# Kernel optimization log

Measured on AMD Instinct MI355X. Metric: run time of the kernel, lower is better.

Reference implementation:

```python
import jax, jax.numpy as jnp
import numpy as np
import math

EPS_T = 1e-3   # temperature floor from `sigmoid(raw)*(1-0.001)+0.001`
EPS_W = 1e-8   # normalization epsilon


def _cdist(a, b):
    # Euclidean distance matrix [N, C], like torch.cdist(p=2).
    a2 = jnp.sum(a * a, axis=-1, keepdims=True)        # [N, 1]
    b2 = jnp.sum(b * b, axis=-1)                       # [C]
    d2 = a2 + b2 - 2.0 * (a @ b.T)                     # [N, C]
    return jnp.sqrt(jnp.maximum(d2, 1e-12))


def setup_inputs() -> dict:
    key = jax.random.key(0)
    k_x, k_p, k_g = jax.random.split(key, 3)
    N, D, C = 262144, 128, 256
    x = jax.random.normal(k_x, (N, D), dtype=jnp.float32)
    prototypes = jax.random.normal(k_p, (C, D), dtype=jnp.float32)
    grid_pos = jax.random.normal(k_g, (C, D), dtype=jnp.float32)
    # logit(0.95) so temperature == init_temperature
    temp_raw = jnp.array([math.log(0.95 / 0.05)], dtype=jnp.float32)
    gate_logits = jnp.zeros((C,), dtype=jnp.float32)
    return {"x": x, "prototypes": prototypes, "grid_pos": grid_pos,
            "temp_raw": temp_raw, "gate_logits": gate_logits}


def reference(x, prototypes, grid_pos, temp_raw, gate_logits):
    temperature = jax.nn.sigmoid(temp_raw)[0] * (1.0 - EPS_T) + EPS_T
    gate = jax.nn.sigmoid(gate_logits)[None, :]            # [1, C]
    d_total = _cdist(x, prototypes) + _cdist(x, grid_pos)  # [N, C]
    w = jnp.exp(-d_total / temperature)
    w = w / (jnp.sum(w, axis=-1, keepdims=True) + EPS_W)
    w = w * gate
    w = w / (jnp.sum(w, axis=-1, keepdims=True) + EPS_W)
    blended = w @ prototypes                               # [N, D]
    return blended, w
```

## Files before the change

### kernel.cpp

```cpp
#include <hip/hip_runtime.h>

typedef short v8s __attribute__((ext_vector_type(8)));
typedef float v4f __attribute__((ext_vector_type(4)));
typedef float f32x16 __attribute__((ext_vector_type(16)));
typedef unsigned int v2u __attribute__((ext_vector_type(2)));
typedef unsigned int v4u __attribute__((ext_vector_type(4)));
typedef unsigned short ushort_t;

#define NC 256
#define ND 128

__device__ __forceinline__ unsigned short f2bf(float f) {
  union { float f; unsigned int u; } v; v.f = f;
  unsigned int u = v.u;
  unsigned int r = (u + 0x7fffu + ((u >> 16) & 1u)) >> 16;
  return (unsigned short)r;
}

__device__ __forceinline__ unsigned int cvt_pk_bf16(float a, float b) {
  unsigned int r;
  asm("v_cvt_pk_bf16_f32 %0, %1, %2" : "=v"(r) : "v"(a), "v"(b));
  return r;
}

__device__ __forceinline__ float bf_lo(unsigned int u) { return __uint_as_float(u << 16); }
__device__ __forceinline__ float bf_hi(unsigned int u) { return __uint_as_float(u & 0xffff0000u); }

__global__ void som_prep_kernel(const float* __restrict__ P, const float* __restrict__ G,
                                const float* __restrict__ gate_logits,
                                ushort_t* __restrict__ PbfA, ushort_t* __restrict__ GbfA,
                                ushort_t* __restrict__ PTbfA,
                                float* __restrict__ b2p, float* __restrict__ b2g,
                                float* __restrict__ gatev) {
  int c = blockIdx.x;
  int t = threadIdx.x;
  float p = P[c * ND + t];
  float g = G[c * ND + t];

  int ct = c >> 5, l31 = c & 31;
  int s = t >> 4, hia = (t >> 3) & 1, j = t & 7;
  int lane = l31 + 32 * hia;
  PbfA[((ct * 8 + s) * 64 + lane) * 8 + j] = f2bf(p);
  GbfA[((ct * 8 + s) * 64 + lane) * 8 + j] = f2bf(g);

  int dt = t >> 5, l31d = t & 31;
  int sc = c >> 4, hic = (c >> 3) & 1, jc = c & 7;
  int laned = l31d + 32 * hic;
  PTbfA[((dt * 16 + sc) * 64 + laned) * 8 + jc] = f2bf(p);

  float pp = p * p, gg = g * g;
  #pragma unroll
  for (int m = 1; m < 64; m <<= 1) { pp += __shfl_xor(pp, m); gg += __shfl_xor(gg, m); }
  __shared__ float sp[2], sg[2];
  if ((t & 63) == 0) { sp[t >> 6] = pp; sg[t >> 6] = gg; }
  __syncthreads();
  if (t == 0) {
    b2p[c] = sp[0] + sp[1];
    b2g[c] = sg[0] + sg[1];
    gatev[c] = 1.f / (1.f + expf(-gate_logits[c]));
  }
}

__global__ __launch_bounds__(256, 2) void som_main_kernel(
    const float* __restrict__ x,
    const ushort_t* __restrict__ PbfA,
    const ushort_t* __restrict__ GbfA,
    const ushort_t* __restrict__ PTbfA,
    const float* __restrict__ b2p,
    const float* __restrict__ b2g,
    const float* __restrict__ gatev,
    const float* __restrict__ temp_raw,
    float* __restrict__ blended_out,
    float* __restrict__ w_out)
{
  __shared__ char smem[65536];
  const int tid  = threadIdx.x;
  const int wid  = tid >> 6;
  const int lane = tid & 63;
  const int l31  = lane & 31;
  const int hi   = lane >> 5;
  const long long R = ((long long)blockIdx.x * 4 + wid) * 32;
  char* wl = smem + wid * 16384;
  const int rsw = (l31 & 7) << 4;

  float traw = temp_raw[0];
  float sgm = 1.f / (1.f + __builtin_amdgcn_exp2f(-traw * 1.44269504f));
  float T = sgm * (1.f - 1e-3f) + 1e-3f;
  float k2 = 1.44269504f / T;

  const float* xr = x + (R + l31) * ND + hi * 8;
  v8s xb[8];
  float a2 = 0.f;
  #pragma unroll
  for (int s = 0; s < 8; ++s) {
    v4f lo = *(const v4f*)(xr + s * 16);
    v4f h4 = *(const v4f*)(xr + s * 16 + 4);
    v4u w;
    w[0] = cvt_pk_bf16(lo[0], lo[1]);
    w[1] = cvt_pk_bf16(lo[2], lo[3]);
    w[2] = cvt_pk_bf16(h4[0], h4[1]);
    w[3] = cvt_pk_bf16(h4[2], h4[3]);
    xb[s] = __builtin_bit_cast(v8s, w);
    #pragma unroll
    for (int j = 0; j < 4; ++j) {
      a2 = fmaf(lo[j], lo[j], a2);
      a2 = fmaf(h4[j], h4[j], a2);
    }
  }
  a2 += __shfl_xor(a2, 32);

  float s1 = 0.f, su = 0.f;
  const ushort_t* pb = PbfA + lane * 8;
  const ushort_t* gb = GbfA + lane * 8;
  #pragma unroll
  for (int ct = 0; ct < 8; ++ct) {
    f32x16 aP, aG;
    #pragma unroll
    for (int i = 0; i < 16; ++i) { aP[i] = 0.f; aG[i] = 0.f; }
    #pragma unroll
    for (int s = 0; s < 8; ++s) {
      v8s ap = *(const v8s*)(pb + (ct * 8 + s) * 512);
      v8s ag = *(const v8s*)(gb + (ct * 8 + s) * 512);
      aP = __builtin_amdgcn_mfma_f32_32x32x16_bf16(ap, xb[s], aP, 0, 0, 0);
      aG = __builtin_amdgcn_mfma_f32_32x32x16_bf16(ag, xb[s], aG, 0, 0, 0);
    }
    #pragma unroll
    for (int q = 0; q < 4; ++q) {
      int c0 = ct * 32 + q * 8 + hi * 4;
      v4f bp = *(const v4f*)(b2p + c0);
      v4f bg = *(const v4f*)(b2g + c0);
      v4f gt = *(const v4f*)(gatev + c0);
      float uf[4];
      #pragma unroll
      for (int j2 = 0; j2 < 4; ++j2) {
        int r = q * 4 + j2;
        float d2a = fmaf(-2.f, aP[r], a2 + bp[j2]);
        float d2b = fmaf(-2.f, aG[r], a2 + bg[j2]);
        float d = __builtin_amdgcn_sqrtf(fmaxf(d2a, 1e-12f))
                + __builtin_amdgcn_sqrtf(fmaxf(d2b, 1e-12f));
        float e = __builtin_amdgcn_exp2f(-d * k2);
        float uu = e * gt[j2];
        s1 += e; su += uu;
        uf[j2] = uu;
      }
      v2u pk;
      pk[0] = cvt_pk_bf16(uf[0], uf[1]);
      pk[1] = cvt_pk_bf16(uf[2], uf[3]);
      *(v2u*)(wl + l31 * 512 + ((ct * 64 + q * 16 + hi * 8) ^ rsw)) = pk;
    }
  }
  s1 += __shfl_xor(s1, 32);
  su += __shfl_xor(su, 32);
  float scale = 1.f / (su + 1e-8f * (s1 + 1e-8f));

  #pragma unroll
  for (int p = 0; p < 4; ++p) {
    int row = (lane >> 3) + 8 * p;
    float rsc = __shfl(scale, row);
    float* wdst = w_out + (size_t)(R + row) * NC + (lane & 7) * 4;
    #pragma unroll
    for (int ch = 0; ch < 8; ++ch) {
      v2u pk = *(const v2u*)(wl + row * 512 + ((ch * 64 + (lane & 7) * 8) ^ ((row & 7) << 4)));
      v4f wv;
      wv[0] = bf_lo(pk[0]) * rsc;
      wv[1] = bf_hi(pk[0]) * rsc;
      wv[2] = bf_lo(pk[1]) * rsc;
      wv[3] = bf_hi(pk[1]) * rsc;
      *(v4f*)(wdst + ch * 32) = wv;
    }
  }

  f32x16 acc[4];
  #pragma unroll
  for (int dt = 0; dt < 4; ++dt)
    #pragma unroll
    for (int i = 0; i < 16; ++i) acc[dt][i] = 0.f;

  const ushort_t* tb = PTbfA + lane * 8;
  #pragma unroll
  for (int s2 = 0; s2 < 16; ++s2) {
    v4u bw = *(const v4u*)(wl + l31 * 512 + ((s2 * 32 + hi * 16) ^ rsw));
    v8s bfrag = __builtin_bit_cast(v8s, bw);
    #pragma unroll
    for (int dt = 0; dt < 4; ++dt) {
      v8s pa = *(const v8s*)(tb + (dt * 16 + s2) * 512);
      acc[dt] = __builtin_amdgcn_mfma_f32_32x32x16_bf16(pa, bfrag, acc[dt], 0, 0, 0);
    }
  }

  #pragma unroll
  for (int dt = 0; dt < 4; ++dt) {
    #pragma unroll
    for (int q = 0; q < 4; ++q) {
      v4f ov;
      ov[0] = acc[dt][4 * q + 0] * scale;
      ov[1] = acc[dt][4 * q + 1] * scale;
      ov[2] = acc[dt][4 * q + 2] * scale;
      ov[3] = acc[dt][4 * q + 3] * scale;
      *(v4f*)(wl + l31 * 512 + ((dt * 128 + q * 32 + hi * 16) ^ rsw)) = ov;
    }
  }
  #pragma unroll
  for (int p = 0; p < 4; ++p) {
    int row = (lane >> 3) + 8 * p;
    float* bdst = blended_out + (size_t)(R + row) * ND + (lane & 7) * 4;
    #pragma unroll
    for (int ch = 0; ch < 4; ++ch) {
      v4f bv = *(const v4f*)(wl + row * 512 + ((ch * 128 + (lane & 7) * 16) ^ ((row & 7) << 4)));
      *(v4f*)(bdst + ch * 32) = bv;
    }
  }
}

extern "C" void kernel_launch(void* const* d_in, const int* in_sizes, int n_in,
                              void* d_out, int out_size, void* d_ws, size_t ws_size,
                              hipStream_t stream) {
  const float* x    = (const float*)d_in[0];
  const float* P    = (const float*)d_in[1];
  const float* G    = (const float*)d_in[2];
  const float* traw = (const float*)d_in[3];
  const float* gl   = (const float*)d_in[4];
  const int N = in_sizes[0] / ND;

  char* ws = (char*)d_ws;
  ushort_t* PbfA  = (ushort_t*)(ws);
  ushort_t* GbfA  = (ushort_t*)(ws + 65536);
  ushort_t* PTbfA = (ushort_t*)(ws + 131072);
  float* b2p   = (float*)(ws + 196608);
  float* b2g   = (float*)(ws + 197632);
  float* gatev = (float*)(ws + 198656);

  float* blended = (float*)d_out;
  float* wout    = blended + (size_t)N * ND;

  som_prep_kernel<<<NC, ND, 0, stream>>>(P, G, gl, PbfA, GbfA, PTbfA, b2p, b2g, gatev);
  som_main_kernel<<<N / 128, 256, 0, stream>>>(x, PbfA, GbfA, PTbfA, b2p, b2g, gatev,
                                               traw, blended, wout);
}
```

Measured before the change: 152.3 us.

## Switch to 16x16x32 MFMA tiles with 16 rows per wave for higher occupancy

```diff
diff --git a/kernel.cpp b/kernel.cpp
--- a/kernel.cpp
+++ b/kernel.cpp
@@ -2,13 +2,13 @@
 
 typedef short v8s __attribute__((ext_vector_type(8)));
 typedef float v4f __attribute__((ext_vector_type(4)));
-typedef float f32x16 __attribute__((ext_vector_type(16)));
 typedef unsigned int v2u __attribute__((ext_vector_type(2)));
 typedef unsigned int v4u __attribute__((ext_vector_type(4)));
 typedef unsigned short ushort_t;
 
 #define NC 256
 #define ND 128
+#define ROW_B 528
 
 __device__ __forceinline__ unsigned short f2bf(float f) {
   union { float f; unsigned int u; } v; v.f = f;
@@ -37,16 +37,20 @@
   float p = P[c * ND + t];
   float g = G[c * ND + t];
 
-  int ct = c >> 5, l31 = c & 31;
-  int s = t >> 4, hia = (t >> 3) & 1, j = t & 7;
-  int lane = l31 + 32 * hia;
-  PbfA[((ct * 8 + s) * 64 + lane) * 8 + j] = f2bf(p);
-  GbfA[((ct * 8 + s) * 64 + lane) * 8 + j] = f2bf(g);
-
-  int dt = t >> 5, l31d = t & 31;
-  int sc = c >> 4, hic = (c >> 3) & 1, jc = c & 7;
-  int laned = l31d + 32 * hic;
-  PTbfA[((dt * 16 + sc) * 64 + laned) * 8 + jc] = f2bf(p);
+  {
+    int ct = c >> 4, l15 = c & 15;
+    int s = t >> 5, q4 = (t >> 3) & 3, j = t & 7;
+    int lane = l15 + 16 * q4;
+    int idx = ((ct * 4 + s) * 64 + lane) * 8 + j;
+    PbfA[idx] = f2bf(p);
+    GbfA[idx] = f2bf(g);
+  }
+  {
+    int dt = t >> 4, l15 = t & 15;
+    int s2 = c >> 5, q4 = (c >> 3) & 3, j = c & 7;
+    int lane = l15 + 16 * q4;
+    PTbfA[((dt * 8 + s2) * 64 + lane) * 8 + j] = f2bf(p);
+  }
 
   float pp = p * p, gg = g * g;
   #pragma unroll
@@ -61,7 +65,7 @@
   }
 }
 
-__global__ __launch_bounds__(256, 2) void som_main_kernel(
+__global__ __launch_bounds__(256, 4) void som_main_kernel(
     const float* __restrict__ x,
     const ushort_t* __restrict__ PbfA,
     const ushort_t* __restrict__ GbfA,
@@ -73,28 +77,27 @@
     float* __restrict__ blended_out,
     float* __restrict__ w_out)
 {
-  __shared__ char smem[65536];
+  __shared__ char smem[4 * 16 * ROW_B];
   const int tid  = threadIdx.x;
   const int wid  = tid >> 6;
   const int lane = tid & 63;
-  const int l31  = lane & 31;
-  const int hi   = lane >> 5;
-  const long long R = ((long long)blockIdx.x * 4 + wid) * 32;
-  char* wl = smem + wid * 16384;
-  const int rsw = (l31 & 7) << 4;
+  const int l15  = lane & 15;
+  const int q4   = lane >> 4;
+  const long long R = ((long long)blockIdx.x * 4 + wid) * 16;
+  char* wl = smem + wid * 16 * ROW_B;
 
   float traw = temp_raw[0];
   float sgm = 1.f / (1.f + __builtin_amdgcn_exp2f(-traw * 1.44269504f));
   float T = sgm * (1.f - 1e-3f) + 1e-3f;
   float k2 = 1.44269504f / T;
 
-  const float* xr = x + (R + l31) * ND + hi * 8;
-  v8s xb[8];
+  const float* xr = x + (R + l15) * ND + q4 * 8;
+  v8s xb[4];
   float a2 = 0.f;
   #pragma unroll
-  for (int s = 0; s < 8; ++s) {
-    v4f lo = *(const v4f*)(xr + s * 16);
-    v4f h4 = *(const v4f*)(xr + s * 16 + 4);
+  for (int s = 0; s < 4; ++s) {
+    v4f lo = *(const v4f*)(xr + s * 32);
+    v4f h4 = *(const v4f*)(xr + s * 32 + 4);
     v4u w;
     w[0] = cvt_pk_bf16(lo[0], lo[1]);
     w[1] = cvt_pk_bf16(lo[2], lo[3]);
@@ -107,108 +110,94 @@
       a2 = fmaf(h4[j], h4[j], a2);
     }
   }
+  a2 += __shfl_xor(a2, 16);
   a2 += __shfl_xor(a2, 32);
 
   float s1 = 0.f, su = 0.f;
   const ushort_t* pb = PbfA + lane * 8;
   const ushort_t* gb = GbfA + lane * 8;
   #pragma unroll
-  for (int ct = 0; ct < 8; ++ct) {
-    f32x16 aP, aG;
-    #pragma unroll
-    for (int i = 0; i < 16; ++i) { aP[i] = 0.f; aG[i] = 0.f; }
-    #pragma unroll
-    for (int s = 0; s < 8; ++s) {
-      v8s ap = *(const v8s*)(pb + (ct * 8 + s) * 512);
-      v8s ag = *(const v8s*)(gb + (ct * 8 + s) * 512);
-      aP = __builtin_amdgcn_mfma_f32_32x32x16_bf16(ap, xb[s], aP, 0, 0, 0);
-      aG = __builtin_amdgcn_mfma_f32_32x32x16_bf16(ag, xb[s], aG, 0, 0, 0);
-    }
-    #pragma unroll
-    for (int q = 0; q < 4; ++q) {
-      int c0 = ct * 32 + q * 8 + hi * 4;
-      v4f bp = *(const v4f*)(b2p + c0);
-      v4f bg = *(const v4f*)(b2g + c0);
-      v4f gt = *(const v4f*)(gatev + c0);
-      float uf[4];
-      #pragma unroll
-      for (int j2 = 0; j2 < 4; ++j2) {
-        int r = q * 4 + j2;
-        float d2a = fmaf(-2.f, aP[r], a2 + bp[j2]);
-        float d2b = fmaf(-2.f, aG[r], a2 + bg[j2]);
-        float d = __builtin_amdgcn_sqrtf(fmaxf(d2a, 1e-12f))
-                + __builtin_amdgcn_sqrtf(fmaxf(d2b, 1e-12f));
-        float e = __builtin_amdgcn_exp2f(-d * k2);
-        float uu = e * gt[j2];
-        s1 += e; su += uu;
-        uf[j2] = uu;
-      }
-      v2u pk;
-      pk[0] = cvt_pk_bf16(uf[0], uf[1]);
-      pk[1] = cvt_pk_bf16(uf[2], uf[3]);
-      *(v2u*)(wl + l31 * 512 + ((ct * 64 + q * 16 + hi * 8) ^ rsw)) = pk;
-    }
-  }
-  s1 += __shfl_xor(s1, 32);
-  su += __shfl_xor(su, 32);
+  for (int ct = 0; ct < 16; ++ct) {
+    v4f aP = {0.f,0.f,0.f,0.f}, aG = {0.f,0.f,0.f,0.f};
+    #pragma unroll
+    for (int s = 0; s < 4; ++s) {
+      v8s ap = *(const v8s*)(pb + (ct * 4 + s) * 512);
+      v8s ag = *(const v8s*)(gb + (ct * 4 + s) * 512);
+      aP = __builtin_amdgcn_mfma_f32_16x16x32_bf16(ap, xb[s], aP, 0, 0, 0);
+      aG = __builtin_amdgcn_mfma_f32_16x16x32_bf16(ag, xb[s], aG, 0, 0, 0);
+    }
+    int c0 = ct * 16 + q4 * 4;
+    v4f bp = *(const v4f*)(b2p + c0);
+    v4f bg = *(const v4f*)(b2g + c0);
+    v4f gt = *(const v4f*)(gatev + c0);
+    float uf[4];
+    #pragma unroll
+    for (int r = 0; r < 4; ++r) {
+      float d2a = fmaf(-2.f, aP[r], a2 + bp[r]);
+      float d2b = fmaf(-2.f, aG[r], a2 + bg[r]);
+      float d = __builtin_amdgcn_sqrtf(fmaxf(d2a, 1e-12f))
+              + __builtin_amdgcn_sqrtf(fmaxf(d2b, 1e-12f));
+      float e = __builtin_amdgcn_exp2f(-d * k2);
+      float uu = e * gt[r];
+      s1 += e; su += uu;
+      uf[r] = uu;
+    }
+    v2u pk;
+    pk[0] = cvt_pk_bf16(uf[0], uf[1]);
+    pk[1] = cvt_pk_bf16(uf[2], uf[3]);
+    *(v2u*)(wl + l15 * ROW_B + ct * 32 + q4 * 8) = pk;
+  }
+  s1 += __shfl_xor(s1, 16); s1 += __shfl_xor(s1, 32);
+  su += __shfl_xor(su, 16); su += __shfl_xor(su, 32);
   float scale = 1.f / (su + 1e-8f * (s1 + 1e-8f));
 
-  #pragma unroll
-  for (int p = 0; p < 4; ++p) {
-    int row = (lane >> 3) + 8 * p;
-    float rsc = __shfl(scale, row);
-    float* wdst = w_out + (size_t)(R + row) * NC + (lane & 7) * 4;
-    #pragma unroll
-    for (int ch = 0; ch < 8; ++ch) {
-      v2u pk = *(const v2u*)(wl + row * 512 + ((ch * 64 + (lane & 7) * 8) ^ ((row & 7) << 4)));
-      v4f wv;
-      wv[0] = bf_lo(pk[0]) * rsc;
-      wv[1] = bf_hi(pk[0]) * rsc;
-      wv[2] = bf_lo(pk[1]) * rsc;
-      wv[3] = bf_hi(pk[1]) * rsc;
-      *(v4f*)(wdst + ch * 32) = wv;
-    }
-  }
-
-  f32x16 acc[4];
-  #pragma unroll
-  for (int dt = 0; dt < 4; ++dt)
-    #pragma unroll
-    for (int i = 0; i < 16; ++i) acc[dt][i] = 0.f;
-
+  const int erow = lane >> 2;
+  const int ek   = lane & 3;
+  float rsc = __shfl(scale, erow);
+  float* wdst = w_out + (size_t)(R + erow) * NC + ek * 8;
+  #pragma unroll
+  for (int ch = 0; ch < 8; ++ch) {
+    v4u pk = *(const v4u*)(wl + erow * ROW_B + ch * 64 + ek * 16);
+    v4f w0, w1;
+    w0[0] = bf_lo(pk[0]) * rsc; w0[1] = bf_hi(pk[0]) * rsc;
+    w0[2] = bf_lo(pk[1]) * rsc; w0[3] = bf_hi(pk[1]) * rsc;
+    w1[0] = bf_lo(pk[2]) * rsc; w1[1] = bf_hi(pk[2]) * rsc;
+    w1[2] = bf_lo(pk[3]) * rsc; w1[3] = bf_hi(pk[3]) * rsc;
+    *(v4f*)(wdst + ch * 32)     = w0;
+    *(v4f*)(wdst + ch * 32 + 4) = w1;
+  }
+
+  v4f acc[8];
+  #pragma unroll
+  for (int dt = 0; dt < 8; ++dt) acc[dt] = (v4f){0.f,0.f,0.f,0.f};
   const ushort_t* tb = PTbfA + lane * 8;
   #pragma unroll
-  for (int s2 = 0; s2 < 16; ++s2) {
-    v4u bw = *(const v4u*)(wl + l31 * 512 + ((s2 * 32 + hi * 16) ^ rsw));
+  for (int s2 = 0; s2 < 8; ++s2) {
+    v4u bw = *(const v4u*)(wl + l15 * ROW_B + s2 * 64 + q4 * 16);
     v8s bfrag = __builtin_bit_cast(v8s, bw);
     #pragma unroll
-    for (int dt = 0; dt < 4; ++dt) {
-      v8s pa = *(const v8s*)(tb + (dt * 16 + s2) * 512);
-      acc[dt] = __builtin_amdgcn_mfma_f32_32x32x16_bf16(pa, bfrag, acc[dt], 0, 0, 0);
-    }
-  }
-
-  #pragma unroll
-  for (int dt = 0; dt < 4; ++dt) {
-    #pragma unroll
-    for (int q = 0; q < 4; ++q) {
-      v4f ov;
-      ov[0] = acc[dt][4 * q + 0] * scale;
-      ov[1] = acc[dt][4 * q + 1] * scale;
-      ov[2] = acc[dt][4 * q + 2] * scale;
-      ov[3] = acc[dt][4 * q + 3] * scale;
-      *(v4f*)(wl + l31 * 512 + ((dt * 128 + q * 32 + hi * 16) ^ rsw)) = ov;
-    }
-  }
-  #pragma unroll
-  for (int p = 0; p < 4; ++p) {
-    int row = (lane >> 3) + 8 * p;
-    float* bdst = blended_out + (size_t)(R + row) * ND + (lane & 7) * 4;
-    #pragma unroll
-    for (int ch = 0; ch < 4; ++ch) {
-      v4f bv = *(const v4f*)(wl + row * 512 + ((ch * 128 + (lane & 7) * 16) ^ ((row & 7) << 4)));
-      *(v4f*)(bdst + ch * 32) = bv;
-    }
+    for (int dt = 0; dt < 8; ++dt) {
+      v8s pa = *(const v8s*)(tb + (dt * 8 + s2) * 512);
+      acc[dt] = __builtin_amdgcn_mfma_f32_16x16x32_bf16(pa, bfrag, acc[dt], 0, 0, 0);
+    }
+  }
+
+  #pragma unroll
+  for (int dt = 0; dt < 8; ++dt) {
+    v4f ov;
+    ov[0] = acc[dt][0] * scale;
+    ov[1] = acc[dt][1] * scale;
+    ov[2] = acc[dt][2] * scale;
+    ov[3] = acc[dt][3] * scale;
+    *(v4f*)(wl + l15 * ROW_B + dt * 64 + q4 * 16) = ov;
+  }
+  float* bdst = blended_out + (size_t)(R + erow) * ND + ek * 8;
+  #pragma unroll
+  for (int ch = 0; ch < 4; ++ch) {
+    v4f b0 = *(const v4f*)(wl + erow * ROW_B + ch * 128 + ek * 32);
+    v4f b1 = *(const v4f*)(wl + erow * ROW_B + ch * 128 + ek * 32 + 16);
+    *(v4f*)(bdst + ch * 32)     = b0;
+    *(v4f*)(bdst + ch * 32 + 4) = b1;
   }
 }
 
@@ -234,6 +223,6 @@
   float* wout    = blended + (size_t)N * ND;
 
   som_prep_kernel<<<NC, ND, 0, stream>>>(P, G, gl, PbfA, GbfA, PTbfA, b2p, b2g, gatev);
-  som_main_kernel<<<N / 128, 256, 0, stream>>>(x, PbfA, GbfA, PTbfA, b2p, b2g, gatev,
-                                               traw, blended, wout);
-}
+  som_main_kernel<<<N / 64, 256, 0, stream>>>(x, PbfA, GbfA, PTbfA, b2p, b2g, gatev,
+                                              traw, blended, wout);
+}
```

After: 211.3 us. +38.7%, slower.

## Split each 32-row tile across a wave pair to double waves per block

Applied to the files above, without the earlier changes.

```diff
diff --git a/kernel.cpp b/kernel.cpp
--- a/kernel.cpp
+++ b/kernel.cpp
@@ -61,7 +61,7 @@
   }
 }
 
-__global__ __launch_bounds__(256, 2) void som_main_kernel(
+__global__ __launch_bounds__(512, 4) void som_main_kernel(
     const float* __restrict__ x,
     const ushort_t* __restrict__ PbfA,
     const ushort_t* __restrict__ GbfA,
@@ -73,14 +73,17 @@
     float* __restrict__ blended_out,
     float* __restrict__ w_out)
 {
-  __shared__ char smem[65536];
+  __shared__ char smem[4 * 16384 + 2048];
   const int tid  = threadIdx.x;
   const int wid  = tid >> 6;
+  const int pair = wid >> 1;
+  const int h    = wid & 1;
   const int lane = tid & 63;
   const int l31  = lane & 31;
   const int hi   = lane >> 5;
-  const long long R = ((long long)blockIdx.x * 4 + wid) * 32;
-  char* wl = smem + wid * 16384;
+  const long long R = ((long long)blockIdx.x * 4 + pair) * 32;
+  char* wl = smem + pair * 16384;
+  float* sums = (float*)(smem + 65536) + pair * 128;
   const int rsw = (l31 & 7) << 4;
 
   float traw = temp_raw[0];
@@ -113,7 +116,8 @@
   const ushort_t* pb = PbfA + lane * 8;
   const ushort_t* gb = GbfA + lane * 8;
   #pragma unroll
-  for (int ct = 0; ct < 8; ++ct) {
+  for (int ct8 = 0; ct8 < 4; ++ct8) {
+    const int ct = h * 4 + ct8;
     f32x16 aP, aG;
     #pragma unroll
     for (int i = 0; i < 16; ++i) { aP[i] = 0.f; aG[i] = 0.f; }
@@ -151,11 +155,19 @@
   }
   s1 += __shfl_xor(s1, 32);
   su += __shfl_xor(su, 32);
-  float scale = 1.f / (su + 1e-8f * (s1 + 1e-8f));
-
-  #pragma unroll
-  for (int p = 0; p < 4; ++p) {
-    int row = (lane >> 3) + 8 * p;
+  if (hi == 0) {
+    sums[h * 64 + l31]      = s1;
+    sums[h * 64 + 32 + l31] = su;
+  }
+  __syncthreads();
+
+  float s1t = sums[l31] + sums[64 + l31];
+  float sut = sums[32 + l31] + sums[96 + l31];
+  float scale = 1.f / (sut + 1e-8f * (s1t + 1e-8f));
+
+  #pragma unroll
+  for (int pp = 0; pp < 2; ++pp) {
+    int row = (lane >> 3) + 8 * (2 * h + pp);
     float rsc = __shfl(scale, row);
     float* wdst = w_out + (size_t)(R + row) * NC + (lane & 7) * 4;
     #pragma unroll
@@ -170,11 +182,11 @@
     }
   }
 
-  f32x16 acc[4];
-  #pragma unroll
-  for (int dt = 0; dt < 4; ++dt)
-    #pragma unroll
-    for (int i = 0; i < 16; ++i) acc[dt][i] = 0.f;
+  f32x16 acc[2];
+  #pragma unroll
+  for (int dt2 = 0; dt2 < 2; ++dt2)
+    #pragma unroll
+    for (int i = 0; i < 16; ++i) acc[dt2][i] = 0.f;
 
   const ushort_t* tb = PTbfA + lane * 8;
   #pragma unroll
@@ -182,27 +194,32 @@
     v4u bw = *(const v4u*)(wl + l31 * 512 + ((s2 * 32 + hi * 16) ^ rsw));
     v8s bfrag = __builtin_bit_cast(v8s, bw);
     #pragma unroll
-    for (int dt = 0; dt < 4; ++dt) {
-      v8s pa = *(const v8s*)(tb + (dt * 16 + s2) * 512);
-      acc[dt] = __builtin_amdgcn_mfma_f32_32x32x16_bf16(pa, bfrag, acc[dt], 0, 0, 0);
-    }
-  }
-
-  #pragma unroll
-  for (int dt = 0; dt < 4; ++dt) {
+    for (int dt2 = 0; dt2 < 2; ++dt2) {
+      int dtg = h * 2 + dt2;
+      v8s pa = *(const v8s*)(tb + (dtg * 16 + s2) * 512);
+      acc[dt2] = __builtin_amdgcn_mfma_f32_32x32x16_bf16(pa, bfrag, acc[dt2], 0, 0, 0);
+    }
+  }
+  __syncthreads();
+
+  #pragma unroll
+  for (int dt2 = 0; dt2 < 2; ++dt2) {
+    int dtg = h * 2 + dt2;
     #pragma unroll
     for (int q = 0; q < 4; ++q) {
       v4f ov;
-      ov[0] = acc[dt][4 * q + 0] * scale;
-      ov[1] = acc[dt][4 * q + 1] * scale;
-      ov[2] = acc[dt][4 * q + 2] * scale;
-      ov[3] = acc[dt][4 * q + 3] * scale;
-      *(v4f*)(wl + l31 * 512 + ((dt * 128 + q * 32 + hi * 16) ^ rsw)) = ov;
-    }
-  }
-  #pragma unroll
-  for (int p = 0; p < 4; ++p) {
-    int row = (lane >> 3) + 8 * p;
+      ov[0] = acc[dt2][4 * q + 0] * scale;
+      ov[1] = acc[dt2][4 * q + 1] * scale;
+      ov[2] = acc[dt2][4 * q + 2] * scale;
+      ov[3] = acc[dt2][4 * q + 3] * scale;
+      *(v4f*)(wl + l31 * 512 + ((dtg * 128 + q * 32 + hi * 16) ^ rsw)) = ov;
+    }
+  }
+  __syncthreads();
+
+  #pragma unroll
+  for (int pp = 0; pp < 2; ++pp) {
+    int row = (lane >> 3) + 8 * (2 * h + pp);
     float* bdst = blended_out + (size_t)(R + row) * ND + (lane & 7) * 4;
     #pragma unroll
     for (int ch = 0; ch < 4; ++ch) {
@@ -234,6 +251,6 @@
   float* wout    = blended + (size_t)N * ND;
 
   som_prep_kernel<<<NC, ND, 0, stream>>>(P, G, gl, PbfA, GbfA, PTbfA, b2p, b2g, gatev);
-  som_main_kernel<<<N / 128, 256, 0, stream>>>(x, PbfA, GbfA, PTbfA, b2p, b2g, gatev,
+  som_main_kernel<<<N / 128, 512, 0, stream>>>(x, PbfA, GbfA, PTbfA, b2p, b2g, gatev,
                                                traw, blended, wout);
 }
```

Measured after the change: 165.3 us. +8.5%, slower.

## Recompute distance GEMM in two passes to shrink LDS and raise occupancy

Applied to the files above, without the earlier changes.

```diff
diff --git a/kernel.cpp b/kernel.cpp
--- a/kernel.cpp
+++ b/kernel.cpp
@@ -3,12 +3,12 @@
 typedef short v8s __attribute__((ext_vector_type(8)));
 typedef float v4f __attribute__((ext_vector_type(4)));
 typedef float f32x16 __attribute__((ext_vector_type(16)));
-typedef unsigned int v2u __attribute__((ext_vector_type(2)));
 typedef unsigned int v4u __attribute__((ext_vector_type(4)));
 typedef unsigned short ushort_t;
 
 #define NC 256
 #define ND 128
+#define LROW 36
 
 __device__ __forceinline__ unsigned short f2bf(float f) {
   union { float f; unsigned int u; } v; v.f = f;
@@ -23,8 +23,9 @@
   return r;
 }
 
-__device__ __forceinline__ float bf_lo(unsigned int u) { return __uint_as_float(u << 16); }
-__device__ __forceinline__ float bf_hi(unsigned int u) { return __uint_as_float(u & 0xffff0000u); }
+__device__ __forceinline__ void plane32swap(unsigned int &a, unsigned int &b) {
+  asm("v_permlane32_swap_b32 %0, %1" : "+v"(a), "+v"(b));
+}
 
 __global__ void som_prep_kernel(const float* __restrict__ P, const float* __restrict__ G,
                                 const float* __restrict__ gate_logits,
@@ -61,7 +62,7 @@
   }
 }
 
-__global__ __launch_bounds__(256, 2) void som_main_kernel(
+__global__ __launch_bounds__(256, 3) void som_main_kernel(
     const float* __restrict__ x,
     const ushort_t* __restrict__ PbfA,
     const ushort_t* __restrict__ GbfA,
@@ -73,15 +74,16 @@
     float* __restrict__ blended_out,
     float* __restrict__ w_out)
 {
-  __shared__ char smem[65536];
+  __shared__ float smem[4 * 32 * LROW];
   const int tid  = threadIdx.x;
   const int wid  = tid >> 6;
   const int lane = tid & 63;
   const int l31  = lane & 31;
   const int hi   = lane >> 5;
   const long long R = ((long long)blockIdx.x * 4 + wid) * 32;
-  char* wl = smem + wid * 16384;
-  const int rsw = (l31 & 7) << 4;
+  float* wl = smem + wid * 32 * LROW;
+  const int erow = lane >> 3;
+  const int eseg = lane & 7;
 
   float traw = temp_raw[0];
   float sgm = 1.f / (1.f + __builtin_amdgcn_exp2f(-traw * 1.44269504f));
@@ -109,9 +111,10 @@
   }
   a2 += __shfl_xor(a2, 32);
 
-  float s1 = 0.f, su = 0.f;
   const ushort_t* pb = PbfA + lane * 8;
   const ushort_t* gb = GbfA + lane * 8;
+
+  float s1 = 0.f, su = 0.f;
   #pragma unroll
   for (int ct = 0; ct < 8; ++ct) {
     f32x16 aP, aG;
@@ -124,6 +127,58 @@
       aP = __builtin_amdgcn_mfma_f32_32x32x16_bf16(ap, xb[s], aP, 0, 0, 0);
       aG = __builtin_amdgcn_mfma_f32_32x32x16_bf16(ag, xb[s], aG, 0, 0, 0);
     }
+    #pragma unroll
+    for (int q = 0; q < 4; ++q) {
+      int c0 = ct * 32 + q * 8 + hi * 4;
+      v4f bp = *(const v4f*)(b2p + c0);
+      v4f bg = *(const v4f*)(b2g + c0);
+      v4f gt = *(const v4f*)(gatev + c0);
+      #pragma unroll
+      for (int j2 = 0; j2 < 4; ++j2) {
+        int r = q * 4 + j2;
+        float d2a = fmaf(-2.f, aP[r], a2 + bp[j2]);
+        float d2b = fmaf(-2.f, aG[r], a2 + bg[j2]);
+        float d = __builtin_amdgcn_sqrtf(fmaxf(d2a, 1e-12f))
+                + __builtin_amdgcn_sqrtf(fmaxf(d2b, 1e-12f));
+        float e = __builtin_amdgcn_exp2f(-d * k2);
+        s1 += e;
+        su = fmaf(e, gt[j2], su);
+      }
+    }
+  }
+  s1 += __shfl_xor(s1, 32);
+  su += __shfl_xor(su, 32);
+  float scale = 1.f / (su + 1e-8f * (s1 + 1e-8f));
+
+  #pragma unroll
+  for (int s = 0; s < 8; ++s) {
+    v4u t = __builtin_bit_cast(v4u, xb[s]);
+    unsigned int t0 = t[0], t1 = t[1], t2 = t[2], t3 = t[3];
+    asm volatile("" : "+v"(t0), "+v"(t1), "+v"(t2), "+v"(t3));
+    t[0] = t0; t[1] = t1; t[2] = t2; t[3] = t3;
+    xb[s] = __builtin_bit_cast(v8s, t);
+  }
+
+  f32x16 acc[4];
+  #pragma unroll
+  for (int dt = 0; dt < 4; ++dt)
+    #pragma unroll
+    for (int i = 0; i < 16; ++i) acc[dt][i] = 0.f;
+  const ushort_t* tb = PTbfA + lane * 8;
+
+  #pragma unroll
+  for (int ct = 0; ct < 8; ++ct) {
+    f32x16 aP, aG;
+    #pragma unroll
+    for (int i = 0; i < 16; ++i) { aP[i] = 0.f; aG[i] = 0.f; }
+    #pragma unroll
+    for (int s = 0; s < 8; ++s) {
+      v8s ap = *(const v8s*)(pb + (ct * 8 + s) * 512);
+      v8s ag = *(const v8s*)(gb + (ct * 8 + s) * 512);
+      aP = __builtin_amdgcn_mfma_f32_32x32x16_bf16(ap, xb[s], aP, 0, 0, 0);
+      aG = __builtin_amdgcn_mfma_f32_32x32x16_bf16(ag, xb[s], aG, 0, 0, 0);
+    }
+    unsigned int w8[8];
     #pragma unroll
     for (int q = 0; q < 4; ++q) {
       int c0 = ct * 32 + q * 8 + hi * 4;
@@ -139,52 +194,34 @@
         float d = __builtin_amdgcn_sqrtf(fmaxf(d2a, 1e-12f))
                 + __builtin_amdgcn_sqrtf(fmaxf(d2b, 1e-12f));
         float e = __builtin_amdgcn_exp2f(-d * k2);
-        float uu = e * gt[j2];
-        s1 += e; su += uu;
-        uf[j2] = uu;
+        uf[j2] = e * gt[j2];
       }
-      v2u pk;
-      pk[0] = cvt_pk_bf16(uf[0], uf[1]);
-      pk[1] = cvt_pk_bf16(uf[2], uf[3]);
-      *(v2u*)(wl + l31 * 512 + ((ct * 64 + q * 16 + hi * 8) ^ rsw)) = pk;
-    }
-  }
-  s1 += __shfl_xor(s1, 32);
-  su += __shfl_xor(su, 32);
-  float scale = 1.f / (su + 1e-8f * (s1 + 1e-8f));
-
-  #pragma unroll
-  for (int p = 0; p < 4; ++p) {
-    int row = (lane >> 3) + 8 * p;
-    float rsc = __shfl(scale, row);
-    float* wdst = w_out + (size_t)(R + row) * NC + (lane & 7) * 4;
-    #pragma unroll
-    for (int ch = 0; ch < 8; ++ch) {
-      v2u pk = *(const v2u*)(wl + row * 512 + ((ch * 64 + (lane & 7) * 8) ^ ((row & 7) << 4)));
+      w8[2 * q]     = cvt_pk_bf16(uf[0], uf[1]);
+      w8[2 * q + 1] = cvt_pk_bf16(uf[2], uf[3]);
       v4f wv;
-      wv[0] = bf_lo(pk[0]) * rsc;
-      wv[1] = bf_hi(pk[0]) * rsc;
-      wv[2] = bf_lo(pk[1]) * rsc;
-      wv[3] = bf_hi(pk[1]) * rsc;
-      *(v4f*)(wdst + ch * 32) = wv;
-    }
-  }
-
-  f32x16 acc[4];
-  #pragma unroll
-  for (int dt = 0; dt < 4; ++dt)
-    #pragma unroll
-    for (int i = 0; i < 16; ++i) acc[dt][i] = 0.f;
-
-  const ushort_t* tb = PTbfA + lane * 8;
-  #pragma unroll
-  for (int s2 = 0; s2 < 16; ++s2) {
-    v4u bw = *(const v4u*)(wl + l31 * 512 + ((s2 * 32 + hi * 16) ^ rsw));
-    v8s bfrag = __builtin_bit_cast(v8s, bw);
-    #pragma unroll
-    for (int dt = 0; dt < 4; ++dt) {
-      v8s pa = *(const v8s*)(tb + (dt * 16 + s2) * 512);
-      acc[dt] = __builtin_amdgcn_mfma_f32_32x32x16_bf16(pa, bfrag, acc[dt], 0, 0, 0);
+      wv[0] = uf[0] * scale; wv[1] = uf[1] * scale;
+      wv[2] = uf[2] * scale; wv[3] = uf[3] * scale;
+      *(v4f*)(wl + l31 * LROW + q * 8 + hi * 4) = wv;
+    }
+    #pragma unroll
+    for (int b = 0; b < 2; ++b) {
+      unsigned int p0 = w8[4 * b], p1 = w8[4 * b + 1], p2 = w8[4 * b + 2], p3 = w8[4 * b + 3];
+      plane32swap(p0, p2);
+      plane32swap(p1, p3);
+      v4u bw; bw[0] = p0; bw[1] = p1; bw[2] = p2; bw[3] = p3;
+      v8s bfrag = __builtin_bit_cast(v8s, bw);
+      int s2 = 2 * ct + b;
+      #pragma unroll
+      for (int dt = 0; dt < 4; ++dt) {
+        v8s pa = *(const v8s*)(tb + (dt * 16 + s2) * 512);
+        acc[dt] = __builtin_amdgcn_mfma_f32_32x32x16_bf16(pa, bfrag, acc[dt], 0, 0, 0);
+      }
+    }
+    #pragma unroll
+    for (int p = 0; p < 4; ++p) {
+      int row = erow + 8 * p;
+      v4f wv = *(const v4f*)(wl + row * LROW + eseg * 4);
+      *(v4f*)(w_out + (size_t)(R + row) * NC + ct * 32 + eseg * 4) = wv;
     }
   }
 
@@ -197,17 +234,13 @@
       ov[1] = acc[dt][4 * q + 1] * scale;
       ov[2] = acc[dt][4 * q + 2] * scale;
       ov[3] = acc[dt][4 * q + 3] * scale;
-      *(v4f*)(wl + l31 * 512 + ((dt * 128 + q * 32 + hi * 16) ^ rsw)) = ov;
-    }
-  }
-  #pragma unroll
-  for (int p = 0; p < 4; ++p) {
-    int row = (lane >> 3) + 8 * p;
-    float* bdst = blended_out + (size_t)(R + row) * ND + (lane & 7) * 4;
-    #pragma unroll
-    for (int ch = 0; ch < 4; ++ch) {
-      v4f bv = *(const v4f*)(wl + row * 512 + ((ch * 128 + (lane & 7) * 16) ^ ((row & 7) << 4)));
-      *(v4f*)(bdst + ch * 32) = bv;
+      *(v4f*)(wl + l31 * LROW + q * 8 + hi * 4) = ov;
+    }
+    #pragma unroll
+    for (int p = 0; p < 4; ++p) {
+      int row = erow + 8 * p;
+      v4f bv = *(const v4f*)(wl + row * LROW + eseg * 4);
+      *(v4f*)(blended_out + (size_t)(R + row) * ND + dt * 32 + eseg * 4) = bv;
     }
   }
 }
```

After: 392.3 us. 158% more time.
